# Performance work log

Measured on AMD Instinct MI355X. Metric: run time of the kernel, lower is better.

Reference implementation:

```python
import jax, jax.numpy as jnp
import numpy as np

D_MODEL = 1024
N_HEADS = 16
D_HEAD = D_MODEL // N_HEADS
D_FF = 4096
MAX_ITERS = 2
B, T = 8, 1024
LN_EPS = 1e-5


def _layernorm(x, g, b):
    m = jnp.mean(x, axis=-1, keepdims=True)
    v = jnp.mean(jnp.square(x - m), axis=-1, keepdims=True)
    return (x - m) * jax.lax.rsqrt(v + LN_EPS) * g + b


def setup_inputs() -> dict:
    key = jax.random.key(0)
    ks = jax.random.split(key, 16)
    s = 0.02
    inp = {
        "z": jax.random.normal(ks[0], (B, T, D_MODEL), dtype=jnp.float32),
        # per-head Q/K/V projections stacked over heads: [H, D, Dh], bias [H, Dh]
        "Wq": jax.random.normal(ks[1], (N_HEADS, D_MODEL, D_HEAD), dtype=jnp.float32) * s,
        "bq": jnp.zeros((N_HEADS, D_HEAD), dtype=jnp.float32),
        "Wk": jax.random.normal(ks[2], (N_HEADS, D_MODEL, D_HEAD), dtype=jnp.float32) * s,
        "bk": jnp.zeros((N_HEADS, D_HEAD), dtype=jnp.float32),
        "Wv": jax.random.normal(ks[3], (N_HEADS, D_MODEL, D_HEAD), dtype=jnp.float32) * s,
        "bv": jnp.zeros((N_HEADS, D_HEAD), dtype=jnp.float32),
        "Wo": jax.random.normal(ks[4], (D_MODEL, D_MODEL), dtype=jnp.float32) * s,
        "bo": jnp.zeros((D_MODEL,), dtype=jnp.float32),
        "W1": jax.random.normal(ks[5], (D_MODEL, D_FF), dtype=jnp.float32) * s,
        "b1": jnp.zeros((D_FF,), dtype=jnp.float32),
        "W2": jax.random.normal(ks[6], (D_FF, D_MODEL), dtype=jnp.float32) * s,
        "b2": jnp.zeros((D_MODEL,), dtype=jnp.float32),
        "g1": jnp.ones((D_MODEL,), dtype=jnp.float32),
        "be1": jnp.zeros((D_MODEL,), dtype=jnp.float32),
        "g2": jnp.ones((D_MODEL,), dtype=jnp.float32),
        "be2": jnp.zeros((D_MODEL,), dtype=jnp.float32),
    }
    return inp


def reference(z, Wq, bq, Wk, bk, Wv, bv, Wo, bo, W1, b1, W2, b2, g1, be1, g2, be2):
    # Controller outputs (alphas/state/aux) are unused by the original forward -> omitted.
    # Dropout is inference-identity.
    scale = 1.0 / jnp.sqrt(jnp.asarray(D_HEAD, dtype=z.dtype))
    z_refined = z
    for _ in range(MAX_ITERS):
        # batched per-head projections: [B,H,T,Dh]
        q = jnp.einsum('btd,hdk->bhtk', z, Wq) + bq[None, :, None, :]
        k = jnp.einsum('btd,hdk->bhtk', z, Wk) + bk[None, :, None, :]
        v = jnp.einsum('btd,hdk->bhtk', z, Wv) + bv[None, :, None, :]
        scores = jnp.einsum('bhtk,bhsk->bhts', q, k) * scale  # [B,H,T,T]
        attn = jax.nn.softmax(scores, axis=-1)
        o = jnp.einsum('bhts,bhsk->bhtk', attn, v)  # [B,H,T,Dh]
        # concat heads in order (matches torch.cat over head list)
        o = jnp.transpose(o, (0, 2, 1, 3)).reshape(z.shape[0], z.shape[1], D_MODEL)
        attn_out = o @ Wo + bo
        z = _layernorm(z + attn_out, g1, be1)
        z_refined = z
        ffn = jnp.maximum(z @ W1 + b1, 0.0) @ W2 + b2
        z = _layernorm(z + ffn, g2, be2)
    return z_refined
```

## Files before the change

kernel.cpp:

```cpp
#include <hip/hip_runtime.h>
#include <hip/hip_bf16.h>

typedef __bf16 bf16t;
typedef bf16t bf16x4 __attribute__((ext_vector_type(4)));
typedef bf16t bf16x8 __attribute__((ext_vector_type(8)));
typedef float f32x4 __attribute__((ext_vector_type(4)));

#define BT 8192
#define TT 1024
#define DM 1024
#define DFF 4096

static __device__ __forceinline__ f32x4 mfma16(bf16x8 a, bf16x8 b, f32x4 c) {
  return __builtin_amdgcn_mfma_f32_16x16x32_bf16(a, b, c, 0, 0, 0);
}
static __device__ __forceinline__ bf16x8 ld8(const bf16t* p0, const bf16t* p1) {
  bf16x4 lo = *(const bf16x4*)p0;
  bf16x4 hi = *(const bf16x4*)p1;
  return __builtin_shufflevector(lo, hi, 0, 1, 2, 3, 4, 5, 6, 7);
}
static __device__ __forceinline__ f32x4 f4zero() {
  f32x4 z = {0.f, 0.f, 0.f, 0.f};
  return z;
}
static __device__ __forceinline__ f32x4 vmax4(f32x4 a, f32x4 b) {
  f32x4 r;
#pragma unroll
  for (int i = 0; i < 4; i++) r[i] = fmaxf(a[i], b[i]);
  return r;
}
static __device__ __forceinline__ void gld16(const bf16t* g, bf16t* l) {
  __builtin_amdgcn_global_load_lds((const __attribute__((address_space(1))) void*)g,
                                   (__attribute__((address_space(3))) void*)l, 16, 0, 0);
}

__global__ __launch_bounds__(256) void cvt_kernel(const float* __restrict__ in,
                                                  bf16t* __restrict__ out, long n) {
  long i = ((long)blockIdx.x * 256 + threadIdx.x) * 4;
  if (i >= n) return;
  f32x4 v = *(const f32x4*)&in[i];
  bf16x4 o = {(bf16t)v[0], (bf16t)v[1], (bf16t)v[2], (bf16t)v[3]};
  *(bf16x4*)&out[i] = o;
}

__global__ __launch_bounds__(256) void tcvt_kernel(const float* __restrict__ in,
                                                   bf16t* __restrict__ out, int M, int N) {
  __shared__ float T[64][65];
  const int t = threadIdx.x;
  const int ty = t >> 6, tx = t & 63;
  const long n0 = (long)blockIdx.x * 64, m0 = (long)blockIdx.y * 64;
#pragma unroll
  for (int p = 0; p < 16; ++p) {
    int a = ty * 16 + p;
    T[a][tx] = in[(m0 + a) * N + n0 + tx];
  }
  __syncthreads();
#pragma unroll
  for (int p = 0; p < 16; ++p) {
    int r = ty * 16 + p;
    out[(n0 + r) * M + m0 + tx] = (bf16t)T[tx][r];
  }
}

__global__ __launch_bounds__(256) void vtrans_kernel(const bf16t* __restrict__ qkv,
                                                     bf16t* __restrict__ vT) {
  __shared__ bf16t T[64][72];
  const int bh = blockIdx.x;
  const int b = bh >> 4, h = bh & 15;
  const int tt = blockIdx.y;
  const int t = threadIdx.x;
  const int ty = t >> 6, tx = t & 63;
  const long srcbase = ((long)b * TT + tt * 64) * 3072 + 2048 + h * 64;
#pragma unroll
  for (int p = 0; p < 16; ++p) {
    int a = ty * 16 + p;
    T[a][tx] = qkv[srcbase + (long)a * 3072 + tx];
  }
  __syncthreads();
  const long dstbase = ((long)bh * 64) * 1024 + tt * 64;
#pragma unroll
  for (int p = 0; p < 16; ++p) {
    int d = ty * 16 + p;
    vT[dstbase + (long)d * 1024 + tx] = T[tx][d];
  }
}

__global__ __launch_bounds__(256) void pack_qkv_t_kernel(const float* __restrict__ Wq,
                                                         const float* __restrict__ Wk,
                                                         const float* __restrict__ Wv,
                                                         bf16t* __restrict__ WT) {
  __shared__ float T[64][65];
  const int bx = blockIdx.x;
  const int sel = bx >> 4, h = bx & 15;
  const float* src = ((sel == 0) ? Wq : (sel == 1) ? Wk : Wv) + (long)h * 65536;
  const long nbase = (long)sel * 1024 + h * 64;
  const long m0 = (long)blockIdx.y * 64;
  const int t = threadIdx.x;
  const int ty = t >> 6, tx = t & 63;
#pragma unroll
  for (int p = 0; p < 16; ++p) {
    int a = ty * 16 + p;
    T[a][tx] = src[(m0 + a) * 64 + tx];
  }
  __syncthreads();
#pragma unroll
  for (int p = 0; p < 16; ++p) {
    int r = ty * 16 + p;
    WT[(nbase + r) * 1024 + m0 + tx] = (bf16t)T[tx][r];
  }
}

__global__ __launch_bounds__(256) void pack_bias_kernel(const float* __restrict__ bq,
                                                        const float* __restrict__ bk,
                                                        const float* __restrict__ bv,
                                                        float* __restrict__ bqkv) {
  int i = blockIdx.x * 256 + threadIdx.x;
  if (i >= 3072) return;
  int sel = i >> 10, c = i & 1023;
  bqkv[i] = ((sel == 0) ? bq : (sel == 1) ? bk : bv)[c];
}

template <int EPI>
__global__ __launch_bounds__(256) void gemm_kernel(
    const bf16t* __restrict__ A, const bf16t* __restrict__ Bt,
    const float* __restrict__ bias, const float* __restrict__ resid,
    void* __restrict__ Cout, int M, int N, int K) {
  __shared__ bf16t As[2 * 128 * 32];
  __shared__ bf16t Bs[2 * 128 * 32];
  const int tid = threadIdx.x;
  const int lane = tid & 63;
  const int wid = tid >> 6;
  const int wr = wid >> 1, wc = wid & 1;
  const int g = lane >> 4, lr = lane & 15;

  const int gy = M >> 7;
  const int nwg = gridDim.x;
  const int chunk = nwg >> 3;
  const int wg = blockIdx.x;
  const int lid = (wg & 7) * chunk + (wg >> 3);
  const int gsz = gy << 3;
  const int group = lid / gsz;
  const int rem = lid - group * gsz;
  const int rr = rem >> 3;
  const int cc = (group << 3) + (rem & 7);
  const long brow = (long)rr * 128;
  const long bcol = (long)cc * 128;

  f32x4 acc[4][4];
#pragma unroll
  for (int i = 0; i < 4; i++)
#pragma unroll
    for (int j = 0; j < 4; j++) acc[i][j] = f4zero();

  const int srow = tid >> 2;
  const int csrc = (tid & 3) ^ ((tid >> 3) & 3);
  const bf16t* gA = &A[(brow + srow) * (long)K + 8 * csrc];
  const bf16t* gB = &Bt[(bcol + srow) * (long)K + 8 * csrc];
  bf16t* lA = As + wid * 512;
  bf16t* lB = Bs + wid * 512;

  const int xsw = ((lr >> 1) & 3) << 3;
  const int ra0 = (4 * g) ^ xsw;
  const int ra1 = (16 + 4 * g) ^ xsw;

  auto stage = [&](int buf, int k0) {
    gld16(gA + k0, lA + buf * 4096);
    gld16(gA + k0 + (long)64 * K, lA + buf * 4096 + 2048);
    gld16(gB + k0, lB + buf * 4096);
    gld16(gB + k0 + (long)64 * K, lB + buf * 4096 + 2048);
  };

  stage(0, 0);
  __syncthreads();

  int cur = 0;
  for (int k0 = 32; k0 < K; k0 += 32) {
    stage(cur ^ 1, k0);
    bf16x8 af[4], bfv[4];
#pragma unroll
    for (int i = 0; i < 4; i++) {
      const bf16t* r = As + cur * 4096 + (wr * 64 + i * 16 + lr) * 32;
      af[i] = ld8(r + ra0, r + ra1);
    }
#pragma unroll
    for (int j = 0; j < 4; j++) {
      const bf16t* c = Bs + cur * 4096 + (wc * 64 + j * 16 + lr) * 32;
      bfv[j] = ld8(c + ra0, c + ra1);
    }
#pragma unroll
    for (int i = 0; i < 4; i++)
#pragma unroll
      for (int j = 0; j < 4; j++) acc[i][j] = mfma16(af[i], bfv[j], acc[i][j]);
    __syncthreads();
    cur ^= 1;
  }
  {
    bf16x8 af[4], bfv[4];
#pragma unroll
    for (int i = 0; i < 4; i++) {
      const bf16t* r = As + cur * 4096 + (wr * 64 + i * 16 + lr) * 32;
      af[i] = ld8(r + ra0, r + ra1);
    }
#pragma unroll
    for (int j = 0; j < 4; j++) {
      const bf16t* c = Bs + cur * 4096 + (wc * 64 + j * 16 + lr) * 32;
      bfv[j] = ld8(c + ra0, c + ra1);
    }
#pragma unroll
    for (int i = 0; i < 4; i++)
#pragma unroll
      for (int j = 0; j < 4; j++) acc[i][j] = mfma16(af[i], bfv[j], acc[i][j]);
  }

#pragma unroll
  for (int j = 0; j < 4; j++) {
    int col = (int)bcol + wc * 64 + j * 16 + lr;
    float bval = bias ? bias[col] : 0.f;
#pragma unroll
    for (int i = 0; i < 4; i++) {
      long row0 = brow + wr * 64 + i * 16 + 4 * g;
#pragma unroll
      for (int r2 = 0; r2 < 4; r2++) {
        long row = row0 + r2;
        float v = acc[i][j][r2] + bval;
        if (EPI == 0) {
          ((bf16t*)Cout)[row * N + col] = (bf16t)v;
        } else if (EPI == 1) {
          ((bf16t*)Cout)[row * N + col] = (bf16t)fmaxf(v, 0.f);
        } else {
          ((float*)Cout)[row * N + col] = v + resid[row * N + col];
        }
      }
    }
  }
}

__global__ __launch_bounds__(256) void attn_kernel(const bf16t* __restrict__ qkv,
                                                   const bf16t* __restrict__ vT,
                                                   bf16t* __restrict__ o) {
  const int bh = blockIdx.x;
  const int b = bh >> 4, h = bh & 15;
  const int qt = blockIdx.y;
  const int tid = threadIdx.x;
  const int lane = tid & 63;
  const int w = tid >> 6;
  const int g = lane >> 4, lr = lane & 15;

  __shared__ bf16t Qs[64 * 64];
  __shared__ bf16t Ks[2][64 * 64];
  __shared__ bf16t Vs[2][64 * 64];

  const long rowbase = (long)b * TT;
  const long qrow0 = rowbase + (long)qt * 64;

  const int srow_in_call = w * 8 + (lane >> 3);
  const int schunk = (lane & 7) ^ ((lane >> 3) & 7);
  const int soff = 8 * schunk;

  const bf16t* qsrc = &qkv[(qrow0 + srow_in_call) * 3072 + h * 64 + soff];
  const bf16t* ksrc = &qkv[(rowbase + srow_in_call) * 3072 + 1024 + h * 64 + soff];
  const bf16t* vsrc = &vT[((long)bh * 64 + srow_in_call) * 1024 + soff];
  bf16t* ldst = (bf16t*)((w * 8) * 64);

  auto stageQ = [&]() {
    gld16(qsrc, Qs + (size_t)ldst);
    gld16(qsrc + (long)32 * 3072, Qs + (size_t)ldst + 32 * 64);
  };
  auto stageK = [&](int buf, int kt) {
    const bf16t* s = ksrc + (long)kt * 64 * 3072;
    gld16(s, Ks[buf] + (size_t)ldst);
    gld16(s + (long)32 * 3072, Ks[buf] + (size_t)ldst + 32 * 64);
  };
  auto stageV = [&](int buf, int kt) {
    const bf16t* s = vsrc + kt * 64;
    gld16(s, Vs[buf] + (size_t)ldst);
    gld16(s + (long)32 * 1024, Vs[buf] + (size_t)ldst + 32 * 64);
  };

  stageQ();
  stageK(0, 0);
  stageV(0, 0);
  __syncthreads();

  const int swk = (lr & 7) << 3;
  const int o0 = (4 * g) ^ swk, o1 = (16 + 4 * g) ^ swk;
  const int o2 = (32 + 4 * g) ^ swk, o3 = (48 + 4 * g) ^ swk;

  const bf16t* qrow = Qs + (w * 16 + lr) * 64;
  const bf16x8 qb_lo = ld8(qrow + o0, qrow + o1);
  const bf16x8 qb_hi = ld8(qrow + o2, qrow + o3);

  f32x4 acc_o[4];
#pragma unroll
  for (int j = 0; j < 4; j++) acc_o[j] = f4zero();
  float mrun = -1e30f, lrun = 0.f;

  int cur = 0;
  for (int kt = 0; kt < 16; ++kt) {
    if (kt < 15) {
      stageK(cur ^ 1, kt + 1);
      stageV(cur ^ 1, kt + 1);
    }

    f32x4 s[4];
#pragma unroll
    for (int jt = 0; jt < 4; jt++) {
      const bf16t* krow = Ks[cur] + (jt * 16 + lr) * 64;
      bf16x8 ka_lo = ld8(krow + o0, krow + o1);
      bf16x8 ka_hi = ld8(krow + o2, krow + o3);
      f32x4 t = f4zero();
      t = mfma16(ka_lo, qb_lo, t);
      t = mfma16(ka_hi, qb_hi, t);
      s[jt] = t;
    }

#pragma unroll
    for (int jt = 0; jt < 4; jt++)
#pragma unroll
      for (int r = 0; r < 4; r++) s[jt][r] *= 0.125f;

    f32x4 mv = vmax4(vmax4(s[0], s[1]), vmax4(s[2], s[3]));
    float tm = fmaxf(fmaxf(mv[0], mv[1]), fmaxf(mv[2], mv[3]));
    tm = fmaxf(tm, __shfl_xor(tm, 16, 64));
    tm = fmaxf(tm, __shfl_xor(tm, 32, 64));

    float mnew = fmaxf(mrun, tm);
    float corr = __expf(mrun - mnew);
    mrun = mnew;

    f32x4 sv = f4zero();
#pragma unroll
    for (int jt = 0; jt < 4; jt++)
#pragma unroll
      for (int r = 0; r < 4; r++) {
        float pv = __expf(s[jt][r] - mnew);
        s[jt][r] = pv;
        sv[r] += pv;
      }
    float tsum = sv[0] + sv[1] + sv[2] + sv[3];
    tsum += __shfl_xor(tsum, 16, 64);
    tsum += __shfl_xor(tsum, 32, 64);
    lrun = lrun * corr + tsum;

#pragma unroll
    for (int r = 0; r < 4; r++) {
      float cq = __shfl(corr, 20 * g + r, 64);
#pragma unroll
      for (int dt = 0; dt < 4; dt++) acc_o[dt][r] *= cq;
    }

    bf16x8 pa0, pa1;
#pragma unroll
    for (int r = 0; r < 4; r++) {
      pa0[r] = (bf16t)s[0][r];
      pa0[r + 4] = (bf16t)s[1][r];
      pa1[r] = (bf16t)s[2][r];
      pa1[r + 4] = (bf16t)s[3][r];
    }

#pragma unroll
    for (int dt = 0; dt < 4; dt++) {
      const bf16t* vrow = Vs[cur] + (dt * 16 + lr) * 64;
      bf16x8 vb_lo = ld8(vrow + o0, vrow + o1);
      bf16x8 vb_hi = ld8(vrow + o2, vrow + o3);
      acc_o[dt] = mfma16(pa0, vb_lo, acc_o[dt]);
      acc_o[dt] = mfma16(pa1, vb_hi, acc_o[dt]);
    }

    __syncthreads();
    cur ^= 1;
  }

  float inv = 1.0f / lrun;
#pragma unroll
  for (int r = 0; r < 4; r++) {
    float iq = __shfl(inv, 20 * g + r, 64);
    long row = qrow0 + w * 16 + 4 * g + r;
#pragma unroll
    for (int dt = 0; dt < 4; dt++) {
      o[row * (long)DM + h * 64 + dt * 16 + lr] = (bf16t)(acc_o[dt][r] * iq);
    }
  }
}

__global__ __launch_bounds__(256) void ln_kernel(const float* __restrict__ x,
                                                 const float* __restrict__ gamma,
                                                 const float* __restrict__ beta,
                                                 bf16t* __restrict__ out_bf,
                                                 float* __restrict__ out_f32) {
  const long row = blockIdx.x;
  const int tid = threadIdx.x;
  const float* xr = x + row * DM;
  f32x4 v = *(const f32x4*)&xr[tid * 4];
  float s = v[0] + v[1] + v[2] + v[3];
  float ss = v[0] * v[0] + v[1] * v[1] + v[2] * v[2] + v[3] * v[3];
#pragma unroll
  for (int m = 1; m < 64; m <<= 1) {
    s += __shfl_xor(s, m, 64);
    ss += __shfl_xor(ss, m, 64);
  }
  __shared__ float red[8];
  const int w = tid >> 6, lane = tid & 63;
  if (lane == 0) {
    red[w] = s;
    red[4 + w] = ss;
  }
  __syncthreads();
  s = red[0] + red[1] + red[2] + red[3];
  ss = red[4] + red[5] + red[6] + red[7];
  float mean = s * (1.f / DM);
  float var = ss * (1.f / DM) - mean * mean;
  float inv = rsqrtf(var + 1e-5f);
  f32x4 ga = *(const f32x4*)&gamma[tid * 4];
  f32x4 be = *(const f32x4*)&beta[tid * 4];
  bf16x4 ob;
  f32x4 of;
#pragma unroll
  for (int c = 0; c < 4; c++) {
    float y = (v[c] - mean) * inv * ga[c] + be[c];
    ob[c] = (bf16t)y;
    of[c] = y;
  }
  long base = row * DM + tid * 4;
  if (out_bf) *(bf16x4*)&out_bf[base] = ob;
  if (out_f32) *(f32x4*)&out_f32[base] = of;
}

extern "C" void kernel_launch(void* const* d_in, const int* in_sizes, int n_in,
                              void* d_out, int out_size, void* d_ws, size_t ws_size,
                              hipStream_t stream) {
  const float* z = (const float*)d_in[0];
  const float* Wq = (const float*)d_in[1];
  const float* bq = (const float*)d_in[2];
  const float* Wk = (const float*)d_in[3];
  const float* bk = (const float*)d_in[4];
  const float* Wv = (const float*)d_in[5];
  const float* bv = (const float*)d_in[6];
  const float* Wo = (const float*)d_in[7];
  const float* bo = (const float*)d_in[8];
  const float* W1 = (const float*)d_in[9];
  const float* b1 = (const float*)d_in[10];
  const float* W2 = (const float*)d_in[11];
  const float* b2 = (const float*)d_in[12];
  const float* g1 = (const float*)d_in[13];
  const float* be1 = (const float*)d_in[14];
  const float* g2 = (const float*)d_in[15];
  const float* be2 = (const float*)d_in[16];

  char* p = (char*)d_ws;
  auto alloc = [&](size_t bytes) {
    char* r = p;
    p += (bytes + 255) & ~(size_t)255;
    return r;
  };
  bf16t* wqkvT = (bf16t*)alloc((size_t)3072 * 1024 * 2);
  float* bqkv = (float*)alloc((size_t)3072 * 4);
  bf16t* woT = (bf16t*)alloc((size_t)1024 * 1024 * 2);
  bf16t* w1T = (bf16t*)alloc((size_t)4096 * 1024 * 2);
  bf16t* w2T = (bf16t*)alloc((size_t)1024 * 4096 * 2);
  bf16t* act = (bf16t*)alloc((size_t)BT * 1024 * 2);
  bf16t* obuf = (bf16t*)alloc((size_t)BT * 1024 * 2);
  bf16t* big = (bf16t*)alloc((size_t)BT * 4096 * 2);
  float* tbuf = (float*)alloc((size_t)BT * 1024 * 4);
  float* residf = (float*)alloc((size_t)BT * 1024 * 4);
  bf16t* vT = (bf16t*)tbuf;

  pack_qkv_t_kernel<<<dim3(48, 16), dim3(256), 0, stream>>>(Wq, Wk, Wv, wqkvT);
  pack_bias_kernel<<<dim3(12), dim3(256), 0, stream>>>(bq, bk, bv, bqkv);
  tcvt_kernel<<<dim3(16, 16), dim3(256), 0, stream>>>(Wo, woT, 1024, 1024);
  tcvt_kernel<<<dim3(64, 16), dim3(256), 0, stream>>>(W1, w1T, 1024, 4096);
  tcvt_kernel<<<dim3(16, 64), dim3(256), 0, stream>>>(W2, w2T, 4096, 1024);
  cvt_kernel<<<dim3(8192), dim3(256), 0, stream>>>(z, act, (long)BT * 1024);

  for (int iter = 0; iter < 2; ++iter) {
    gemm_kernel<0><<<dim3(1536), dim3(256), 0, stream>>>(
        act, wqkvT, bqkv, (const float*)nullptr, (void*)big, BT, 3072, 1024);
    vtrans_kernel<<<dim3(128, 16), dim3(256), 0, stream>>>(big, vT);
    attn_kernel<<<dim3(128, 16), dim3(256), 0, stream>>>(big, vT, obuf);
    const float* rsrc = (iter == 0) ? z : residf;
    gemm_kernel<2><<<dim3(512), dim3(256), 0, stream>>>(
        obuf, woT, bo, rsrc, (void*)tbuf, BT, 1024, 1024);
    if (iter == 1) {
      ln_kernel<<<dim3(8192), dim3(256), 0, stream>>>(tbuf, g1, be1, (bf16t*)nullptr,
                                                      (float*)d_out);
      break;
    }
    ln_kernel<<<dim3(8192), dim3(256), 0, stream>>>(tbuf, g1, be1, act, residf);
    gemm_kernel<1><<<dim3(2048), dim3(256), 0, stream>>>(
        act, w1T, b1, (const float*)nullptr, (void*)big, BT, 4096, 1024);
    gemm_kernel<2><<<dim3(512), dim3(256), 0, stream>>>(
        big, w2T, b2, residf, (void*)tbuf, BT, 1024, 4096);
    ln_kernel<<<dim3(8192), dim3(256), 0, stream>>>(tbuf, g2, be2, act, residf);
  }
}
```

Before: 696.0 us.

## Triple-buffer GEMM shared-memory pipeline with explicit vmcnt waits

Converts the GEMM main loop from double-buffered LDS staging with a full __syncthreads per step to a three-stage ring buffer that prefetches two tiles ahead. It waits with s_waitcnt vmcnt(4) so only the oldest tile's loads must land before the barrier, letting more global-load latency overlap the MFMA work. The cost is 50% more LDS per block, which may lower occupancy. The fixed vmcnt count also assumes each stage issues exactly four loads per thread.

```diff
diff --git a/kernel.cpp b/kernel.cpp
--- a/kernel.cpp
+++ b/kernel.cpp
@@ -125,8 +125,8 @@
     const bf16t* __restrict__ A, const bf16t* __restrict__ Bt,
     const float* __restrict__ bias, const float* __restrict__ resid,
     void* __restrict__ Cout, int M, int N, int K) {
-  __shared__ bf16t As[2 * 128 * 32];
-  __shared__ bf16t Bs[2 * 128 * 32];
+  __shared__ bf16t As[3 * 128 * 32];
+  __shared__ bf16t Bs[3 * 128 * 32];
   const int tid = threadIdx.x;
   const int lane = tid & 63;
   const int wid = tid >> 6;
@@ -170,46 +170,44 @@
     gld16(gB + k0 + (long)64 * K, lB + buf * 4096 + 2048);
   };
 
+  const int nt = K >> 5;
   stage(0, 0);
-  __syncthreads();
-
-  int cur = 0;
-  for (int k0 = 32; k0 < K; k0 += 32) {
-    stage(cur ^ 1, k0);
+  stage(1, 32);
+  asm volatile("s_waitcnt vmcnt(4)" ::: "memory");
+  __builtin_amdgcn_s_barrier();
+  __builtin_amdgcn_sched_barrier(0);
+
+  for (int t = 0; t < nt; ++t) {
+    const int k2 = (t + 2) << 5;
+    const bool pf = (k2 < K);
+    if (pf) stage((t + 2) % 3, k2);
+
+    const bf16t* bufA = As + (t % 3) * 4096;
+    const bf16t* bufB = Bs + (t % 3) * 4096;
     bf16x8 af[4], bfv[4];
 #pragma unroll
     for (int i = 0; i < 4; i++) {
-      const bf16t* r = As + cur * 4096 + (wr * 64 + i * 16 + lr) * 32;
+      const bf16t* r = bufA + (wr * 64 + i * 16 + lr) * 32;
       af[i] = ld8(r + ra0, r + ra1);
     }
 #pragma unroll
     for (int j = 0; j < 4; j++) {
-      const bf16t* c = Bs + cur * 4096 + (wc * 64 + j * 16 + lr) * 32;
+      const bf16t* c = bufB + (wc * 64 + j * 16 + lr) * 32;
       bfv[j] = ld8(c + ra0, c + ra1);
     }
 #pragma unroll
     for (int i = 0; i < 4; i++)
 #pragma unroll
       for (int j = 0; j < 4; j++) acc[i][j] = mfma16(af[i], bfv[j], acc[i][j]);
-    __syncthreads();
-    cur ^= 1;
-  }
-  {
-    bf16x8 af[4], bfv[4];
-#pragma unroll
-    for (int i = 0; i < 4; i++) {
-      const bf16t* r = As + cur * 4096 + (wr * 64 + i * 16 + lr) * 32;
-      af[i] = ld8(r + ra0, r + ra1);
-    }
-#pragma unroll
-    for (int j = 0; j < 4; j++) {
-      const bf16t* c = Bs + cur * 4096 + (wc * 64 + j * 16 + lr) * 32;
-      bfv[j] = ld8(c + ra0, c + ra1);
-    }
-#pragma unroll
-    for (int i = 0; i < 4; i++)
-#pragma unroll
-      for (int j = 0; j < 4; j++) acc[i][j] = mfma16(af[i], bfv[j], acc[i][j]);
+
+    if (t + 1 < nt) {
+      if (pf)
+        asm volatile("s_waitcnt vmcnt(4)" ::: "memory");
+      else
+        asm volatile("s_waitcnt vmcnt(0)" ::: "memory");
+      __builtin_amdgcn_s_barrier();
+      __builtin_amdgcn_sched_barrier(0);
+    }
   }
 
 #pragma unroll
```

New measurement: 697.2 us. About the same (+0.2%).
